# Kernel tuning notes

Measured on AMD Instinct MI355X. Metric: run time of the kernel, lower is better.

## Reference

```python
import jax, jax.numpy as jnp
import numpy as np

B, A, D = 64, 4096, 512
TOP_K = 5

def setup_inputs() -> dict:
    key = jax.random.key(0)
    k1, k2, k3 = jax.random.split(key, 3)
    s_embed = jax.random.normal(k1, (B, D), dtype=jnp.float32)
    a_embeds = jax.random.normal(k2, (B, A, D), dtype=jnp.float32)
    available_mask = jax.random.randint(k3, (B, A), 0, 2) > 0
    # make sure each row has at least one available action
    available_mask = available_mask.at[:, 0].set(True)
    return {"s_embed": s_embed, "a_embeds": a_embeds,
            "available_mask": available_mask, "alpha": 1}


def reference(s_embed, a_embeds, available_mask, alpha):
    alpha = jnp.float32(alpha)
    # logits[b,a] = <s_embed[b], a_embeds[b,a]>
    logits = jnp.einsum('bd,bad->ba', s_embed, a_embeds)  # [B, A]
    # masked_fill unavailable actions with (global min - 1)
    fill = jnp.min(logits) - 1.0
    logits = jnp.where(available_mask, logits, fill)
    # top-k mask via scatter
    k = min(logits.shape[1], TOP_K)
    _, top_ids = jax.lax.top_k(logits, k)  # [B, k]
    rows = jnp.arange(logits.shape[0])[:, None]
    top_mask = jnp.zeros(logits.shape, dtype=bool).at[rows, top_ids].set(True)
    # temperature softmax (max-shifted, matching the torch code)
    probs = jax.nn.softmax((logits - jnp.max(logits, -1, keepdims=True)) / alpha, axis=-1)
    # keep only available & top-k, renormalize
    keep = available_mask & top_mask
    probs = jnp.where(keep, probs, 0.0)
    probs = probs / jnp.sum(probs, -1, keepdims=True)
    # categorical sample (zeros -> -inf logits, never sampled)
    action = jax.random.categorical(jax.random.key(42), jnp.log(probs), axis=-1)
    return action, logits
```

## Files before the change

kernel.cpp:

```cpp
#include <hip/hip_runtime.h>
#include <cstdint>
#include <cstddef>

#define NB 64
#define NA 4096
#define ND 512

typedef float f32x4 __attribute__((ext_vector_type(4)));

__device__ __forceinline__ unsigned enc_f(float f){
  unsigned b = __float_as_uint(f);
  return (b & 0x80000000u) ? ~b : (b | 0x80000000u);
}
__device__ __forceinline__ float dec_f(unsigned e){
  unsigned b = (e & 0x80000000u) ? (e ^ 0x80000000u) : ~e;
  return __uint_as_float(b);
}

__device__ __forceinline__ unsigned rotl32(unsigned x, int d){ return (x << d) | (x >> (32 - d)); }

__device__ unsigned threefry_bits(unsigned n){
  const unsigned ks0 = 0u;
  const unsigned ks1 = 42u;
  const unsigned ks2 = 0x1BD11BDAu ^ ks0 ^ ks1;
  unsigned x0 = 0u;
  unsigned x1 = n;
  x0 += ks0; x1 += ks1;
  const int r0[4] = {13, 15, 26, 6};
  const int r1[4] = {17, 29, 16, 24};
  #pragma unroll
  for (int j = 0; j < 4; j++){ x0 += x1; x1 = rotl32(x1, r0[j]); x1 ^= x0; }
  x0 += ks1; x1 += ks2 + 1u;
  #pragma unroll
  for (int j = 0; j < 4; j++){ x0 += x1; x1 = rotl32(x1, r1[j]); x1 ^= x0; }
  x0 += ks2; x1 += ks0 + 2u;
  #pragma unroll
  for (int j = 0; j < 4; j++){ x0 += x1; x1 = rotl32(x1, r0[j]); x1 ^= x0; }
  x0 += ks0; x1 += ks1 + 3u;
  #pragma unroll
  for (int j = 0; j < 4; j++){ x0 += x1; x1 = rotl32(x1, r1[j]); x1 ^= x0; }
  x0 += ks1; x1 += ks2 + 4u;
  #pragma unroll
  for (int j = 0; j < 4; j++){ x0 += x1; x1 = rotl32(x1, r0[j]); x1 ^= x0; }
  x0 += ks2; x1 += ks0 + 5u;
  return x0 ^ x1;
}

__global__ void init_ws(unsigned* ws){ ws[threadIdx.x * 16] = 0xFFFFFFFFu; }

__global__ __launch_bounds__(256) void dot_kernel(const float* __restrict__ s,
                                                  const float* __restrict__ ae,
                                                  float* __restrict__ logits,
                                                  unsigned* __restrict__ minw){
  __shared__ unsigned sm[4];
  int wave = threadIdx.x >> 6;
  int lane = threadIdx.x & 63;
  int blk  = blockIdx.x;
  int b = blk >> 10;
  int a = ((blk & 1023) << 2) | wave;
  const float* ar = ae + (size_t)(b * NA + a) * ND;
  const float* sr = s + b * ND;
  f32x4 a0 = __builtin_nontemporal_load((const f32x4*)(ar + lane * 4));
  f32x4 a1 = __builtin_nontemporal_load((const f32x4*)(ar + 256 + lane * 4));
  f32x4 s0 = *(const f32x4*)(sr + lane * 4);
  f32x4 s1 = *(const f32x4*)(sr + 256 + lane * 4);
  float p = a0.x*s0.x + a0.y*s0.y + a0.z*s0.z + a0.w*s0.w
          + a1.x*s1.x + a1.y*s1.y + a1.z*s1.z + a1.w*s1.w;
  #pragma unroll
  for (int off = 32; off > 0; off >>= 1) p += __shfl_xor(p, off, 64);
  if (lane == 0){
    logits[(size_t)b * NA + a] = p;
    sm[wave] = enc_f(p);
  }
  __syncthreads();
  if (threadIdx.x == 0){
    unsigned m01 = sm[0] < sm[1] ? sm[0] : sm[1];
    unsigned m23 = sm[2] < sm[3] ? sm[2] : sm[3];
    unsigned m   = m01 < m23 ? m01 : m23;
    atomicMin(minw + (blk & 255) * 16, m);
  }
}

__global__ __launch_bounds__(256) void row_kernel(float* __restrict__ out,
                                                  const void* __restrict__ maskp,
                                                  const unsigned* __restrict__ ws,
                                                  const unsigned* __restrict__ alpha_raw){
  __shared__ float row[NA];
  __shared__ unsigned su[4];
  __shared__ float rv[4]; __shared__ int ri[4];
  __shared__ float selv[5]; __shared__ int seli[5];
  __shared__ int s_mflag;
  __shared__ float s_fill;
  int b = blockIdx.x;
  int t = threadIdx.x;
  float* lrow = out + NB + (size_t)b * NA;
  const unsigned char* m8  = (const unsigned char*)maskp;
  const unsigned*      m32 = (const unsigned*)maskp;

  if (t == 0) s_mflag = 1;
  __syncthreads();
  for (int i = t; i < 4096; i += 256)
    if (m32[i] > 1u) s_mflag = 0;

  unsigned e = ws[t * 16];
  #pragma unroll
  for (int off = 32; off > 0; off >>= 1){
    unsigned o = __shfl_xor(e, off, 64);
    e = o < e ? o : e;
  }
  if ((t & 63) == 0) su[t >> 6] = e;
  __syncthreads();
  if (t == 0){
    unsigned r01 = su[0] < su[1] ? su[0] : su[1];
    unsigned r23 = su[2] < su[3] ? su[2] : su[3];
    unsigned r   = r01 < r23 ? r01 : r23;
    s_fill = dec_f(r) - 1.0f;
  }
  __syncthreads();
  int   mflag = s_mflag;
  float fill  = s_fill;

  for (int a = t; a < NA; a += 256){
    int idx = b * NA + a;
    bool av = mflag ? (m32[idx] != 0u) : (m8[idx] != 0);
    float v = lrow[a];
    float mv = av ? v : fill;
    row[a]  = mv;
    lrow[a] = mv;
  }
  __syncthreads();

  for (int k = 0; k < 5; k++){
    float bv = -INFINITY; int bi = 0x7FFFFFFF;
    for (int a = t; a < NA; a += 256){
      float v = row[a];
      if (v > bv){ bv = v; bi = a; }
    }
    #pragma unroll
    for (int off = 32; off > 0; off >>= 1){
      float ov = __shfl_xor(bv, off, 64);
      int   oi = __shfl_xor(bi, off, 64);
      if (ov > bv || (ov == bv && oi < bi)){ bv = ov; bi = oi; }
    }
    if ((t & 63) == 0){ rv[t >> 6] = bv; ri[t >> 6] = bi; }
    __syncthreads();
    if (t == 0){
      float fv = rv[0]; int fi = ri[0];
      for (int w = 1; w < 4; w++)
        if (rv[w] > fv || (rv[w] == fv && ri[w] < fi)){ fv = rv[w]; fi = ri[w]; }
      selv[k] = fv; seli[k] = fi;
      row[fi] = -INFINITY;
    }
    __syncthreads();
  }

  if (t == 0){
    unsigned ab = *alpha_raw;
    float alpha = (ab < 0x00800000u) ? (float)(int)ab : __uint_as_float(ab);
    float best = -INFINITY; int ba = 0;
    for (int k = 0; k < 5; k++){
      int idx  = seli[k];
      int gidx = b * NA + idx;
      bool av = mflag ? (m32[gidx] != 0u) : (m8[gidx] != 0);
      if (!av) continue;
      unsigned bits = threefry_bits((unsigned)gidx);
      float f = __uint_as_float((bits >> 9) | 0x3F800000u) - 1.0f;
      const float tiny = 1.17549435e-38f;
      float u = fmaxf(tiny, f + tiny);
      float g = -logf(-logf(u));
      float sc = selv[k] / alpha + g;
      if (sc > best){ best = sc; ba = idx; }
    }
    out[b] = (float)ba;
  }
}

extern "C" void kernel_launch(void* const* d_in, const int* in_sizes, int n_in,
                              void* d_out, int out_size, void* d_ws, size_t ws_size,
                              hipStream_t stream){
  const float*    s     = (const float*)d_in[0];
  const float*    ae    = (const float*)d_in[1];
  const void*     mask  = d_in[2];
  const unsigned* alpha = (const unsigned*)d_in[3];
  float*    out = (float*)d_out;
  unsigned* ws  = (unsigned*)d_ws;

  hipLaunchKernelGGL(init_ws,    dim3(1),           dim3(256), 0, stream, ws);
  hipLaunchKernelGGL(dot_kernel, dim3(NB * NA / 4), dim3(256), 0, stream, s, ae, out + NB, ws);
  hipLaunchKernelGGL(row_kernel, dim3(NB),          dim3(256), 0, stream, out, mask, ws, alpha);
}
```

Baseline: 109.8 us.

## Widen blocks to 1024 threads and keep row top-k values in registers

The dot kernel now runs 16 waves per block (one action per wave), which cuts the block count and the number of atomicMin calls. The row kernel uses 1024 threads, each holding four logits in registers instead of a shared-memory row, and the mask-format detection moves into the init kernel, which stores a flag in the workspace. This removes the per-row mask scan and the shared-memory traffic in the top-k loop. The cost is lower occupancy flexibility for the large-block dot kernel and a broadcast of the winning index after each selection round.

```diff
diff --git a/kernel.cpp b/kernel.cpp
--- a/kernel.cpp
+++ b/kernel.cpp
@@ -7,6 +7,8 @@
 #define ND 512
 
 typedef float f32x4 __attribute__((ext_vector_type(4)));
+
+#define WS_FLAG 4081
 
 __device__ __forceinline__ unsigned enc_f(float f){
   unsigned b = __float_as_uint(f);
@@ -46,18 +48,29 @@
   return x0 ^ x1;
 }
 
-__global__ void init_ws(unsigned* ws){ ws[threadIdx.x * 16] = 0xFFFFFFFFu; }
-
-__global__ __launch_bounds__(256) void dot_kernel(const float* __restrict__ s,
-                                                  const float* __restrict__ ae,
-                                                  float* __restrict__ logits,
-                                                  unsigned* __restrict__ minw){
-  __shared__ unsigned sm[4];
+__global__ __launch_bounds__(256) void init_ws(unsigned* __restrict__ ws,
+                                               const unsigned* __restrict__ m32){
+  __shared__ int bad;
+  int t = threadIdx.x;
+  if (t == 0) bad = 0;
+  ws[t * 16] = 0xFFFFFFFFu;
+  __syncthreads();
+  for (int i = t; i < 4096; i += 256)
+    if (m32[i] > 1u) bad = 1;
+  __syncthreads();
+  if (t == 0) ws[WS_FLAG] = bad ? 0u : 1u;
+}
+
+__global__ __launch_bounds__(1024) void dot_kernel(const float* __restrict__ s,
+                                                   const float* __restrict__ ae,
+                                                   float* __restrict__ logits,
+                                                   unsigned* __restrict__ minw){
+  __shared__ unsigned sm[16];
   int wave = threadIdx.x >> 6;
   int lane = threadIdx.x & 63;
   int blk  = blockIdx.x;
-  int b = blk >> 10;
-  int a = ((blk & 1023) << 2) | wave;
+  int b = blk >> 8;
+  int a = ((blk & 255) << 4) | wave;
   const float* ar = ae + (size_t)(b * NA + a) * ND;
   const float* sr = s + b * ND;
   f32x4 a0 = __builtin_nontemporal_load((const f32x4*)(ar + lane * 4));
@@ -74,35 +87,30 @@
   }
   __syncthreads();
   if (threadIdx.x == 0){
-    unsigned m01 = sm[0] < sm[1] ? sm[0] : sm[1];
-    unsigned m23 = sm[2] < sm[3] ? sm[2] : sm[3];
-    unsigned m   = m01 < m23 ? m01 : m23;
+    unsigned m = sm[0];
+    #pragma unroll
+    for (int w = 1; w < 16; w++) m = sm[w] < m ? sm[w] : m;
     atomicMin(minw + (blk & 255) * 16, m);
   }
 }
 
-__global__ __launch_bounds__(256) void row_kernel(float* __restrict__ out,
-                                                  const void* __restrict__ maskp,
-                                                  const unsigned* __restrict__ ws,
-                                                  const unsigned* __restrict__ alpha_raw){
-  __shared__ float row[NA];
-  __shared__ unsigned su[4];
-  __shared__ float rv[4]; __shared__ int ri[4];
+__global__ __launch_bounds__(1024) void row_kernel(float* __restrict__ out,
+                                                   const void* __restrict__ maskp,
+                                                   const unsigned* __restrict__ ws,
+                                                   const unsigned* __restrict__ alpha_raw){
+  __shared__ unsigned su[16];
+  __shared__ float rv[16]; __shared__ int ri[16];
   __shared__ float selv[5]; __shared__ int seli[5];
-  __shared__ int s_mflag;
+  __shared__ int swin;
   __shared__ float s_fill;
   int b = blockIdx.x;
   int t = threadIdx.x;
   float* lrow = out + NB + (size_t)b * NA;
   const unsigned char* m8  = (const unsigned char*)maskp;
   const unsigned*      m32 = (const unsigned*)maskp;
-
-  if (t == 0) s_mflag = 1;
-  __syncthreads();
-  for (int i = t; i < 4096; i += 256)
-    if (m32[i] > 1u) s_mflag = 0;
-
-  unsigned e = ws[t * 16];
+  int mflag = (int)ws[WS_FLAG];
+
+  unsigned e = (t < 256) ? ws[t * 16] : 0xFFFFFFFFu;
   #pragma unroll
   for (int off = 32; off > 0; off >>= 1){
     unsigned o = __shfl_xor(e, off, 64);
@@ -111,31 +119,36 @@
   if ((t & 63) == 0) su[t >> 6] = e;
   __syncthreads();
   if (t == 0){
-    unsigned r01 = su[0] < su[1] ? su[0] : su[1];
-    unsigned r23 = su[2] < su[3] ? su[2] : su[3];
-    unsigned r   = r01 < r23 ? r01 : r23;
+    unsigned r = su[0];
+    #pragma unroll
+    for (int w = 1; w < 16; w++) r = su[w] < r ? su[w] : r;
     s_fill = dec_f(r) - 1.0f;
   }
   __syncthreads();
-  int   mflag = s_mflag;
-  float fill  = s_fill;
-
-  for (int a = t; a < NA; a += 256){
-    int idx = b * NA + a;
-    bool av = mflag ? (m32[idx] != 0u) : (m8[idx] != 0);
-    float v = lrow[a];
-    float mv = av ? v : fill;
-    row[a]  = mv;
-    lrow[a] = mv;
-  }
-  __syncthreads();
+  float fill = s_fill;
+
+  float v0, v1, v2, v3;
+  {
+    int i0 = b * NA + t;
+    bool a0 = mflag ? (m32[i0] != 0u) : (m8[i0] != 0);
+    bool a1 = mflag ? (m32[i0 + 1024] != 0u) : (m8[i0 + 1024] != 0);
+    bool a2 = mflag ? (m32[i0 + 2048] != 0u) : (m8[i0 + 2048] != 0);
+    bool a3 = mflag ? (m32[i0 + 3072] != 0u) : (m8[i0 + 3072] != 0);
+    v0 = a0 ? lrow[t]        : fill;
+    v1 = a1 ? lrow[t + 1024] : fill;
+    v2 = a2 ? lrow[t + 2048] : fill;
+    v3 = a3 ? lrow[t + 3072] : fill;
+    lrow[t]        = v0;
+    lrow[t + 1024] = v1;
+    lrow[t + 2048] = v2;
+    lrow[t + 3072] = v3;
+  }
 
   for (int k = 0; k < 5; k++){
-    float bv = -INFINITY; int bi = 0x7FFFFFFF;
-    for (int a = t; a < NA; a += 256){
-      float v = row[a];
-      if (v > bv){ bv = v; bi = a; }
-    }
+    float bv = v0; int bi = t;
+    if (v1 > bv){ bv = v1; bi = t + 1024; }
+    if (v2 > bv){ bv = v2; bi = t + 2048; }
+    if (v3 > bv){ bv = v3; bi = t + 3072; }
     #pragma unroll
     for (int off = 32; off > 0; off >>= 1){
       float ov = __shfl_xor(bv, off, 64);
@@ -146,12 +159,17 @@
     __syncthreads();
     if (t == 0){
       float fv = rv[0]; int fi = ri[0];
-      for (int w = 1; w < 4; w++)
+      #pragma unroll
+      for (int w = 1; w < 16; w++)
         if (rv[w] > fv || (rv[w] == fv && ri[w] < fi)){ fv = rv[w]; fi = ri[w]; }
-      selv[k] = fv; seli[k] = fi;
-      row[fi] = -INFINITY;
+      selv[k] = fv; seli[k] = fi; swin = fi;
     }
     __syncthreads();
+    int wi = swin;
+    if (wi == t)            v0 = -INFINITY;
+    else if (wi == t + 1024) v1 = -INFINITY;
+    else if (wi == t + 2048) v2 = -INFINITY;
+    else if (wi == t + 3072) v3 = -INFINITY;
   }
 
   if (t == 0){
@@ -185,7 +203,10 @@
   float*    out = (float*)d_out;
   unsigned* ws  = (unsigned*)d_ws;
 
-  hipLaunchKernelGGL(init_ws,    dim3(1),           dim3(256), 0, stream, ws);
-  hipLaunchKernelGGL(dot_kernel, dim3(NB * NA / 4), dim3(256), 0, stream, s, ae, out + NB, ws);
-  hipLaunchKernelGGL(row_kernel, dim3(NB),          dim3(256), 0, stream, out, mask, ws, alpha);
-}
+  hipLaunchKernelGGL(init_ws,    dim3(1),            dim3(256),  0, stream,
+                     ws, (const unsigned*)mask);
+  hipLaunchKernelGGL(dot_kernel, dim3(NB * NA / 16), dim3(1024), 0, stream,
+                     s, ae, out + NB, ws);
+  hipLaunchKernelGGL(row_kernel, dim3(NB),           dim3(1024), 0, stream,
+                     out, mask, ws, alpha);
+}
```

Result: slower. 115.1 us (+4.8%).
